# Kernel tuning notes

Hardware: AMD Instinct MI355X
Metric: run time of the kernel (lower is better)

The kernel has to match this reference:

```python
import jax, jax.numpy as jnp
import numpy as np

D_STATE = 16

def setup_inputs() -> dict:
    key = jax.random.key(0)
    ks = jax.random.split(key, 7)
    B, L, d_model = 2, 4096, 1024
    d_inner, d_conv, d_state = 2048, 4, D_STATE
    s = 0.02
    return {
        "x": jax.random.normal(ks[0], (B, L, d_model), jnp.float32),
        "W_in": jax.random.normal(ks[1], (2 * d_inner, d_model), jnp.float32) * s,
        "conv_w": jax.random.normal(ks[2], (d_inner, d_conv), jnp.float32) * 0.3,
        "conv_b": jax.random.normal(ks[3], (d_inner,), jnp.float32) * 0.1,
        "W_xproj": jax.random.normal(ks[4], (2 * d_state + d_inner, d_inner), jnp.float32) * s,
        "D": jnp.ones((d_inner,), jnp.float32),
        "W_out": jax.random.normal(ks[5], (d_model, d_inner), jnp.float32) * s,
    }

def _silu(v):
    return v * jax.nn.sigmoid(v)

def reference(x, W_in, conv_w, conv_b, W_xproj, D, W_out):
    Bsz, L, _ = x.shape
    d_inner, d_conv = conv_w.shape
    d_state = D_STATE
    # in_proj -> split into x branch and gate z
    xz = jnp.einsum('bld,ed->ble', x, W_in)           # [B,L,2*d_inner]
    xb, z = xz[..., :d_inner], xz[..., d_inner:]
    # causal depthwise conv1d (left pad d_conv-1, truncate to L)
    xpad = jnp.pad(xb, ((0, 0), (d_conv - 1, 0), (0, 0)))
    xc = conv_b
    for k in range(d_conv):  # tiny fixed kernel loop
        xc = xc + conv_w[:, k] * xpad[:, k:k + L, :]
    xc = _silu(xc)                                    # [B,L,d_inner]
    # x_proj -> B, C, delta
    proj = jnp.einsum('bld,ed->ble', xc, W_xproj)     # [B,L,2*d_state+d_inner]
    Bm = proj[..., :d_state]
    Cm = proj[..., d_state:2 * d_state]
    delta = jax.nn.softplus(proj[..., 2 * d_state:])  # [B,L,d_inner]
    # selective 'scan' as written collapses: y[b,l,d] = delta*x * sum_s B*C + D*x
    bc = jnp.einsum('bls,bls->bl', Bm, Cm)            # [B,L]
    y = delta * xc * bc[..., None] + D * xc
    y = y * _silu(z)
    return jnp.einsum('bld,ed->ble', y, W_out)        # [B,L,d_model]
```

## Files before the change

kernel.cpp:

```cpp
#include <hip/hip_runtime.h>
#include <hip/hip_bf16.h>
#include <cstdint>
#include <cmath>

typedef __bf16 bf16x8 __attribute__((ext_vector_type(8)));
typedef float  f32x4  __attribute__((ext_vector_type(4)));
typedef unsigned short u16x8 __attribute__((ext_vector_type(8)));

#define BT 128
#define BK 64

__device__ __forceinline__ float bf2f(unsigned short h) {
  union { unsigned int u; float f; } v; v.u = ((unsigned int)h) << 16;
  return v.f;
}
__device__ __forceinline__ unsigned short f2bf(float x) {
  union { float f; unsigned int u; } v; v.f = x;
  unsigned int r = v.u + 0x7fffu + ((v.u >> 16) & 1u);
  return (unsigned short)(r >> 16);
}

__device__ __forceinline__ void gld_lds16(const void* g, void* l) {
  __builtin_amdgcn_global_load_lds(
      (const __attribute__((address_space(1))) unsigned int*)g,
      (__attribute__((address_space(3))) unsigned int*)l,
      16, 0, 0);
}

__device__ __forceinline__ void cvt4(const float* __restrict__ in,
                                     unsigned short* __restrict__ out, int i) {
  float4 v = reinterpret_cast<const float4*>(in)[i];
  ushort4 o;
  o.x = f2bf(v.x); o.y = f2bf(v.y); o.z = f2bf(v.z); o.w = f2bf(v.w);
  reinterpret_cast<ushort4*>(out)[i] = o;
}

__global__ void cvt_head(const float* __restrict__ x, unsigned short* __restrict__ xb,
                         const float* __restrict__ W_in, unsigned short* __restrict__ wb) {
  int b = blockIdx.x;
  if (b < 8192) cvt4(x, xb, b * 256 + threadIdx.x);
  else          cvt4(W_in, wb, (b - 8192) * 256 + threadIdx.x);
}

__device__ void conv_strip(const unsigned short* __restrict__ xz,
                           const float* __restrict__ conv_w,
                           const float* __restrict__ conv_b,
                           unsigned short* __restrict__ xc,
                           int strip, int tid) {
  const int bl0  = strip * 32;
  const int seq0 = bl0 & ~4095;
  const int c0   = tid * 8;
  float w[4][8], bb[8];
#pragma unroll
  for (int j = 0; j < 8; ++j) {
    float4 wr = reinterpret_cast<const float4*>(conv_w)[c0 + j];
    w[0][j] = wr.x; w[1][j] = wr.y; w[2][j] = wr.z; w[3][j] = wr.w;
    bb[j] = conv_b[c0 + j];
  }
  float win[3][8];
#pragma unroll
  for (int i = 0; i < 3; ++i) {
    int r = bl0 - 3 + i;
    if (r >= seq0) {
      u16x8 v = *reinterpret_cast<const u16x8*>(xz + (size_t)r * 4096 + c0);
#pragma unroll
      for (int j = 0; j < 8; ++j) win[i][j] = bf2f(v[j]);
    } else {
#pragma unroll
      for (int j = 0; j < 8; ++j) win[i][j] = 0.f;
    }
  }
  for (int i = 0; i < 32; ++i) {
    const int bl = bl0 + i;
    u16x8 v = *reinterpret_cast<const u16x8*>(xz + (size_t)bl * 4096 + c0);
    u16x8 o;
#pragma unroll
    for (int j = 0; j < 8; ++j) {
      float cur = bf2f(v[j]);
      float a = bb[j] + w[0][j] * win[0][j] + w[1][j] * win[1][j]
                      + w[2][j] * win[2][j] + w[3][j] * cur;
      o[j] = f2bf(a / (1.f + expf(-a)));
      win[0][j] = win[1][j]; win[1][j] = win[2][j]; win[2][j] = cur;
    }
    *reinterpret_cast<u16x8*>(xc + (size_t)bl * 2048 + c0) = o;
  }
}

__global__ void mid_fused(const unsigned short* __restrict__ xz,
                          const float* __restrict__ conv_w,
                          const float* __restrict__ conv_b,
                          unsigned short* __restrict__ xc,
                          const float* __restrict__ W_xproj, unsigned short* __restrict__ wx_bf,
                          const float* __restrict__ W_out,   unsigned short* __restrict__ wo_bf) {
  int b = blockIdx.x;
  if (b < 256) { conv_strip(xz, conv_w, conv_b, xc, b, threadIdx.x); return; }
  b -= 256;
  if (b < 4160) { cvt4(W_xproj, wx_bf, b * 256 + threadIdx.x); return; }
  cvt4(W_out, wo_bf, (b - 4160) * 256 + threadIdx.x);
}

template <int GUARD_N, int OUT_F32>
__global__ __launch_bounds__(256, 2)
void gemm_bt(const unsigned short* __restrict__ A,
             const unsigned short* __restrict__ B,
             void* __restrict__ Cv,
             int N, int K, int ldA, int ldB, int ldC)
{
  __shared__ __align__(16) unsigned short sA[BT * BK];
  __shared__ __align__(16) unsigned short sB[BT * BK];

  const int tid  = threadIdx.x;
  const int lane = tid & 63;
  const int wave = tid >> 6;
  const int row0 = blockIdx.x * BT;
  const int col0 = blockIdx.y * BT;

  const int wrow = (wave & 1) * 64;
  const int wcol = (wave >> 1) * 64;
  const int l15  = lane & 15;
  const int q    = lane >> 4;

  f32x4 acc[4][4];
#pragma unroll
  for (int i = 0; i < 4; ++i)
#pragma unroll
    for (int j = 0; j < 4; ++j)
      acc[i][j] = (f32x4){0.f, 0.f, 0.f, 0.f};

  const int nk = K / BK;
  for (int kt = 0; kt < nk; ++kt) {
    const int k0 = kt * BK;
#pragma unroll
    for (int t = 0; t < 4; ++t) {
      int c  = t * 256 + tid;
      int r  = c >> 3;
      int g  = c & 7;
      int gs = (g ^ (r & 7)) * 8;
      gld_lds16(A + (size_t)(row0 + r) * ldA + k0 + gs, (void*)(sA + c * 8));
      int br = col0 + r;
      if (GUARD_N) br = (br < N) ? br : (N - 1);
      gld_lds16(B + (size_t)br * ldB + k0 + gs, (void*)(sB + c * 8));
    }
    __syncthreads();

#pragma unroll
    for (int kk = 0; kk < BK; kk += 32) {
      const int grb = kk >> 3;
      bf16x8 af[4], bfr[4];
#pragma unroll
      for (int i = 0; i < 4; ++i) {
        int ar = wrow + i * 16 + l15;
        af[i] = *reinterpret_cast<const bf16x8*>(
            sA + ar * BK + (((grb + q) ^ (ar & 7)) << 3));
        int br = wcol + i * 16 + l15;
        bfr[i] = *reinterpret_cast<const bf16x8*>(
            sB + br * BK + (((grb + q) ^ (br & 7)) << 3));
      }
#pragma unroll
      for (int i = 0; i < 4; ++i)
#pragma unroll
        for (int j = 0; j < 4; ++j)
          acc[i][j] = __builtin_amdgcn_mfma_f32_16x16x32_bf16(af[i], bfr[j], acc[i][j], 0, 0, 0);
    }
    __syncthreads();
  }

#pragma unroll
  for (int i = 0; i < 4; ++i) {
#pragma unroll
    for (int j = 0; j < 4; ++j) {
      int colw = col0 + wcol + j * 16 + l15;
      if (GUARD_N && colw >= N) continue;
#pragma unroll
      for (int r = 0; r < 4; ++r) {
        int roww = row0 + wrow + i * 16 + q * 4 + r;
        if (OUT_F32)
          ((float*)Cv)[(size_t)roww * ldC + colw] = acc[i][j][r];
        else
          ((unsigned short*)Cv)[(size_t)roww * ldC + colw] = f2bf(acc[i][j][r]);
      }
    }
  }
}

#define BARX() do { __builtin_amdgcn_sched_barrier(0); \
                    __builtin_amdgcn_s_barrier(); \
                    __builtin_amdgcn_sched_barrier(0); } while (0)
#define VMW(n) asm volatile("s_waitcnt vmcnt(" #n ")" ::: "memory")

#define STAGE_A(b, h, kt) do { \
  const unsigned short* _p = Ab + (size_t)((h) * 128) * ldA + (kt) * 64; \
  gld_lds16(_p,                     (void*)&sA[b][((h) * 128      + rr) * 64 + (g8 << 3)]); \
  gld_lds16(_p + (size_t)64 * ldA,  (void*)&sA[b][((h) * 128 + 64 + rr) * 64 + (g8 << 3)]); \
} while (0)

#define STAGE_B(b, h, kt) do { \
  const unsigned short* _p = Bb + (size_t)((h) * 128) * ldB + (kt) * 64; \
  gld_lds16(_p,                     (void*)&sB[b][((h) * 128      + rr) * 64 + (g8 << 3)]); \
  gld_lds16(_p + (size_t)64 * ldB,  (void*)&sB[b][((h) * 128 + 64 + rr) * 64 + (g8 << 3)]); \
} while (0)

#define RD_A(b, p) do { \
  af[0][0] = *reinterpret_cast<const bf16x8*>(&sA[b][aOff + (2*(p)    ) * 1024 + kph0]); \
  af[0][1] = *reinterpret_cast<const bf16x8*>(&sA[b][aOff + (2*(p)    ) * 1024 + kph1]); \
  af[1][0] = *reinterpret_cast<const bf16x8*>(&sA[b][aOff + (2*(p) + 1) * 1024 + kph0]); \
  af[1][1] = *reinterpret_cast<const bf16x8*>(&sA[b][aOff + (2*(p) + 1) * 1024 + kph1]); \
} while (0)

#define RD_B(b) do { \
  bf[0][0] = *reinterpret_cast<const bf16x8*>(&sB[b][bOff + 0 * 1024 + kph0]); \
  bf[0][1] = *reinterpret_cast<const bf16x8*>(&sB[b][bOff + 0 * 1024 + kph1]); \
  bf[1][0] = *reinterpret_cast<const bf16x8*>(&sB[b][bOff + 1 * 1024 + kph0]); \
  bf[1][1] = *reinterpret_cast<const bf16x8*>(&sB[b][bOff + 1 * 1024 + kph1]); \
  bf[2][0] = *reinterpret_cast<const bf16x8*>(&sB[b][bOff + 2 * 1024 + kph0]); \
  bf[2][1] = *reinterpret_cast<const bf16x8*>(&sB[b][bOff + 2 * 1024 + kph1]); \
  bf[3][0] = *reinterpret_cast<const bf16x8*>(&sB[b][bOff + 3 * 1024 + kph0]); \
  bf[3][1] = *reinterpret_cast<const bf16x8*>(&sB[b][bOff + 3 * 1024 + kph1]); \
} while (0)

#define MM2(i, j) \
  acc[i][j] = __builtin_amdgcn_mfma_f32_16x16x32_bf16(af[(i) & 1][0], bf[j][0], acc[i][j], 0, 0, 0); \
  acc[i][j] = __builtin_amdgcn_mfma_f32_16x16x32_bf16(af[(i) & 1][1], bf[j][1], acc[i][j], 0, 0, 0)

#define MFMA_PH(p) do { \
  __builtin_amdgcn_s_setprio(1); \
  MM2(2*(p),     0); MM2(2*(p),     1); MM2(2*(p),     2); MM2(2*(p),     3); \
  MM2(2*(p) + 1, 0); MM2(2*(p) + 1, 1); MM2(2*(p) + 1, 2); MM2(2*(p) + 1, 3); \
  __builtin_amdgcn_s_setprio(0); \
} while (0)

__global__ __launch_bounds__(512, 2)
void gemm256(const unsigned short* __restrict__ A,
             const unsigned short* __restrict__ B,
             unsigned short* __restrict__ C,
             int K, int ldA, int ldB, int ldC, int nbn)
{
  __shared__ __align__(16) unsigned short sA[2][256 * 64];
  __shared__ __align__(16) unsigned short sB[2][256 * 64];

  const int tid  = threadIdx.x;
  const int lane = tid & 63;
  const int wave = tid >> 6;
  const int wm = wave >> 2;
  const int wn = wave & 3;
  const int l15 = lane & 15;
  const int q   = lane >> 4;

  const int nwg = gridDim.x;
  const int wg  = blockIdx.x;
  const int swz = (wg & 7) * (nwg >> 3) + (wg >> 3);
  const int row0 = (swz / nbn) * 256;
  const int col0 = (swz % nbn) * 256;

  const int rr  = tid >> 3;
  const int g8  = tid & 7;
  const int gsw = ((g8 ^ (rr & 7)) << 3);
  const unsigned short* Ab = A + (size_t)(row0 + rr) * ldA + gsw;
  const unsigned short* Bb = B + (size_t)(col0 + rr) * ldB + gsw;

  const int aOff = (wm * 128 + l15) * 64;
  const int bOff = (wn * 64  + l15) * 64;
  const int a7   = l15 & 7;
  const int kph0 = ((q       ^ a7) << 3);
  const int kph1 = (((4 + q) ^ a7) << 3);

  f32x4 acc[8][4];
#pragma unroll
  for (int i = 0; i < 8; ++i)
#pragma unroll
    for (int j = 0; j < 4; ++j)
      acc[i][j] = (f32x4){0.f, 0.f, 0.f, 0.f};

  bf16x8 af[2][2], bf[4][2];

  const int nk = K >> 6;
  STAGE_A(0, 0, 0); STAGE_A(0, 1, 0);
  STAGE_B(0, 0, 0); STAGE_B(0, 1, 0);
  STAGE_B(1, 0, 1); STAGE_B(1, 1, 1);
  VMW(4);
  BARX();

  const int niter = K >> 7;
  for (int it = 0; it < niter; ++it) {
    const int kt1 = 2 * it + 1;
    int ktE = 2 * it + 2; if (ktE > nk - 1) ktE = nk - 1;
    int ktO = 2 * it + 3; if (ktO > nk - 1) ktO = nk - 1;

    RD_B(0); RD_A(0, 0); STAGE_A(1, 0, kt1);
    BARX(); MFMA_PH(0); BARX();
    RD_A(0, 1); STAGE_A(1, 1, kt1);
    BARX(); MFMA_PH(1); BARX();
    RD_A(0, 2); STAGE_B(0, 0, ktE);
    BARX(); MFMA_PH(2); BARX();
    RD_A(0, 3); STAGE_B(0, 1, ktE);
    VMW(4);
    BARX(); MFMA_PH(3); BARX();

    RD_B(1); RD_A(1, 0); STAGE_A(0, 0, ktE);
    BARX(); MFMA_PH(0); BARX();
    RD_A(1, 1); STAGE_A(0, 1, ktE);
    BARX(); MFMA_PH(1); BARX();
    RD_A(1, 2); STAGE_B(1, 0, ktO);
    BARX(); MFMA_PH(2); BARX();
    RD_A(1, 3); STAGE_B(1, 1, ktO);
    VMW(4);
    BARX(); MFMA_PH(3); BARX();
  }

#pragma unroll
  for (int i = 0; i < 8; ++i) {
    const int roww = row0 + wm * 128 + i * 16 + q * 4;
#pragma unroll
    for (int j = 0; j < 4; ++j) {
      const int colw = col0 + wn * 64 + j * 16 + l15;
      unsigned short* cp = C + (size_t)roww * ldC + colw;
#pragma unroll
      for (int r = 0; r < 4; ++r)
        cp[(size_t)r * ldC] = f2bf(acc[i][j][r]);
    }
  }
}

__global__ __launch_bounds__(256)
void proj_strip(const unsigned short* __restrict__ xc,
                const unsigned short* __restrict__ wx,
                unsigned short* __restrict__ proj)
{
  __shared__ float red[4][32 * 32];
  const int tid  = threadIdx.x;
  const int lane = tid & 63;
  const int wave = tid >> 6;
  const int l15  = lane & 15;
  const int q    = lane >> 4;
  const int row0 = blockIdx.x * 32;

  f32x4 acc[2][2];
#pragma unroll
  for (int i = 0; i < 2; ++i)
#pragma unroll
    for (int j = 0; j < 2; ++j) acc[i][j] = (f32x4){0.f, 0.f, 0.f, 0.f};

  const int kbase = wave * 512;
#pragma unroll 4
  for (int kk = 0; kk < 512; kk += 32) {
    const int k = kbase + kk + q * 8;
    bf16x8 a0 = *reinterpret_cast<const bf16x8*>(&xc[(size_t)(row0 + l15) * 2048 + k]);
    bf16x8 a1 = *reinterpret_cast<const bf16x8*>(&xc[(size_t)(row0 + 16 + l15) * 2048 + k]);
    bf16x8 b0 = *reinterpret_cast<const bf16x8*>(&wx[(size_t)(l15) * 2048 + k]);
    bf16x8 b1 = *reinterpret_cast<const bf16x8*>(&wx[(size_t)(16 + l15) * 2048 + k]);
    acc[0][0] = __builtin_amdgcn_mfma_f32_16x16x32_bf16(a0, b0, acc[0][0], 0, 0, 0);
    acc[0][1] = __builtin_amdgcn_mfma_f32_16x16x32_bf16(a0, b1, acc[0][1], 0, 0, 0);
    acc[1][0] = __builtin_amdgcn_mfma_f32_16x16x32_bf16(a1, b0, acc[1][0], 0, 0, 0);
    acc[1][1] = __builtin_amdgcn_mfma_f32_16x16x32_bf16(a1, b1, acc[1][1], 0, 0, 0);
  }

#pragma unroll
  for (int i = 0; i < 2; ++i)
#pragma unroll
    for (int j = 0; j < 2; ++j)
#pragma unroll
      for (int r = 0; r < 4; ++r)
        red[wave][(i * 16 + q * 4 + r) * 32 + j * 16 + l15] = acc[i][j][r];
  __syncthreads();

#pragma unroll
  for (int t = 0; t < 4; ++t) {
    int idx = tid + t * 256;
    float s = red[0][idx] + red[1][idx] + red[2][idx] + red[3][idx];
    proj[(size_t)(row0 + (idx >> 5)) * 2080 + (idx & 31)] = f2bf(s);
  }
}

__global__ void gate_kernel(const unsigned short* __restrict__ proj,
                            const unsigned short* __restrict__ xz,
                            const float* __restrict__ Dw,
                            unsigned short* __restrict__ xc_y)
{
  const int bl = blockIdx.x;
  const unsigned short* p = proj + (size_t)bl * 2080;
  u16x8 pb0 = *reinterpret_cast<const u16x8*>(p);
  u16x8 pb1 = *reinterpret_cast<const u16x8*>(p + 8);
  u16x8 pc0 = *reinterpret_cast<const u16x8*>(p + 16);
  u16x8 pc1 = *reinterpret_cast<const u16x8*>(p + 24);
  float bc = 0.f;
#pragma unroll
  for (int s = 0; s < 8; ++s)
    bc += bf2f(pb0[s]) * bf2f(pc0[s]) + bf2f(pb1[s]) * bf2f(pc1[s]);

  const int c0 = threadIdx.x * 8;
  u16x8 dv  = *reinterpret_cast<const u16x8*>(p + 32 + c0);
  u16x8 xcv = *reinterpret_cast<const u16x8*>(xc_y + (size_t)bl * 2048 + c0);
  u16x8 zv  = *reinterpret_cast<const u16x8*>(xz + (size_t)bl * 4096 + 2048 + c0);
  float4 d0 = reinterpret_cast<const float4*>(Dw)[c0 / 4];
  float4 d1 = reinterpret_cast<const float4*>(Dw)[c0 / 4 + 1];
  const float* dd0 = reinterpret_cast<const float*>(&d0);
  const float* dd1 = reinterpret_cast<const float*>(&d1);

  u16x8 o;
#pragma unroll
  for (int j = 0; j < 8; ++j) {
    float d = bf2f(dv[j]);
    float delta = (d > 15.f) ? d : log1pf(expf(d));
    float xv = bf2f(xcv[j]);
    float z  = bf2f(zv[j]);
    float Dj = (j < 4) ? dd0[j] : dd1[j - 4];
    float y = delta * xv * bc + Dj * xv;
    y *= z / (1.f + expf(-z));
    o[j] = f2bf(y);
  }
  *reinterpret_cast<u16x8*>(xc_y + (size_t)bl * 2048 + c0) = o;
}

extern "C" void kernel_launch(void* const* d_in, const int* in_sizes, int n_in,
                              void* d_out, int out_size, void* d_ws, size_t ws_size,
                              hipStream_t stream) {
  const float* x       = (const float*)d_in[0];
  const float* W_in    = (const float*)d_in[1];
  const float* conv_w  = (const float*)d_in[2];
  const float* conv_b  = (const float*)d_in[3];
  const float* W_xproj = (const float*)d_in[4];
  const float* Dw      = (const float*)d_in[5];
  const float* W_out   = (const float*)d_in[6];
  float* out = (float*)d_out;

  unsigned short* xz_bf   = (unsigned short*)d_ws;
  unsigned short* xc_bf   = xz_bf  + (size_t)8192 * 4096;
  unsigned short* proj_bf = xc_bf  + (size_t)8192 * 2048;
  unsigned short* xb_bf   = proj_bf + (size_t)8192 * 2080;
  unsigned short* w_bf    = xb_bf  + (size_t)8192 * 1024;

  cvt_head<<<8192 + 4096, 256, 0, stream>>>(x, xb_bf, W_in, w_bf);
  gemm256<<<512, 512, 0, stream>>>(xb_bf, w_bf, xz_bf, 1024, 1024, 1024, 4096, 16);
  mid_fused<<<256 + 4160 + 2048, 256, 0, stream>>>(xz_bf, conv_w, conv_b, xc_bf,
                                                   W_xproj, xb_bf, W_out, w_bf);
  proj_strip<<<256, 256, 0, stream>>>(xc_bf, xb_bf, proj_bf);
  gemm256<<<256, 512, 0, stream>>>(xc_bf, xb_bf + (size_t)32 * 2048, proj_bf + 32,
                                   2048, 2048, 2048, 2080, 8);
  gate_kernel<<<8192, 256, 0, stream>>>(proj_bf, xz_bf, Dw, xc_bf);
  gemm_bt<0, 1><<<dim3(64, 8), 256, 0, stream>>>(xc_bf, w_bf, out, 1024, 2048, 2048, 2048, 1024);
}
```

Before: 393.4 us.

## Double-buffer MFMA register fragments to overlap LDS reads with MFMA phases

Splits the A and B register fragments into even/odd sets so that the LDS reads for the next phase are issued right after the current phase's MFMAs, rather than before them. The intent is to hide LDS read latency behind matrix math. It also reorders the MFMAs so both k-halves interleave across accumulators. This costs more VGPRs under a 512-thread, 2-block launch bound, and adds a prologue read before the loop. The final iteration's prefetch reads stale or unused data, which should be harmless.

```diff
diff --git a/kernel.cpp b/kernel.cpp
--- a/kernel.cpp
+++ b/kernel.cpp
@@ -200,32 +200,37 @@
   gld_lds16(_p + (size_t)64 * ldB,  (void*)&sB[b][((h) * 128 + 64 + rr) * 64 + (g8 << 3)]); \
 } while (0)
 
-#define RD_A(b, p) do { \
-  af[0][0] = *reinterpret_cast<const bf16x8*>(&sA[b][aOff + (2*(p)    ) * 1024 + kph0]); \
-  af[0][1] = *reinterpret_cast<const bf16x8*>(&sA[b][aOff + (2*(p)    ) * 1024 + kph1]); \
-  af[1][0] = *reinterpret_cast<const bf16x8*>(&sA[b][aOff + (2*(p) + 1) * 1024 + kph0]); \
-  af[1][1] = *reinterpret_cast<const bf16x8*>(&sA[b][aOff + (2*(p) + 1) * 1024 + kph1]); \
+#define RD_A_SET(dst, b, p) do { \
+  dst[0][0] = *reinterpret_cast<const bf16x8*>(&sA[b][aOff + (2*(p)    ) * 1024 + kph0]); \
+  dst[0][1] = *reinterpret_cast<const bf16x8*>(&sA[b][aOff + (2*(p)    ) * 1024 + kph1]); \
+  dst[1][0] = *reinterpret_cast<const bf16x8*>(&sA[b][aOff + (2*(p) + 1) * 1024 + kph0]); \
+  dst[1][1] = *reinterpret_cast<const bf16x8*>(&sA[b][aOff + (2*(p) + 1) * 1024 + kph1]); \
 } while (0)
 
-#define RD_B(b) do { \
-  bf[0][0] = *reinterpret_cast<const bf16x8*>(&sB[b][bOff + 0 * 1024 + kph0]); \
-  bf[0][1] = *reinterpret_cast<const bf16x8*>(&sB[b][bOff + 0 * 1024 + kph1]); \
-  bf[1][0] = *reinterpret_cast<const bf16x8*>(&sB[b][bOff + 1 * 1024 + kph0]); \
-  bf[1][1] = *reinterpret_cast<const bf16x8*>(&sB[b][bOff + 1 * 1024 + kph1]); \
-  bf[2][0] = *reinterpret_cast<const bf16x8*>(&sB[b][bOff + 2 * 1024 + kph0]); \
-  bf[2][1] = *reinterpret_cast<const bf16x8*>(&sB[b][bOff + 2 * 1024 + kph1]); \
-  bf[3][0] = *reinterpret_cast<const bf16x8*>(&sB[b][bOff + 3 * 1024 + kph0]); \
-  bf[3][1] = *reinterpret_cast<const bf16x8*>(&sB[b][bOff + 3 * 1024 + kph1]); \
+#define RD_B_SET(dst, b) do { \
+  dst[0][0] = *reinterpret_cast<const bf16x8*>(&sB[b][bOff + 0 * 1024 + kph0]); \
+  dst[0][1] = *reinterpret_cast<const bf16x8*>(&sB[b][bOff + 0 * 1024 + kph1]); \
+  dst[1][0] = *reinterpret_cast<const bf16x8*>(&sB[b][bOff + 1 * 1024 + kph0]); \
+  dst[1][1] = *reinterpret_cast<const bf16x8*>(&sB[b][bOff + 1 * 1024 + kph1]); \
+  dst[2][0] = *reinterpret_cast<const bf16x8*>(&sB[b][bOff + 2 * 1024 + kph0]); \
+  dst[2][1] = *reinterpret_cast<const bf16x8*>(&sB[b][bOff + 2 * 1024 + kph1]); \
+  dst[3][0] = *reinterpret_cast<const bf16x8*>(&sB[b][bOff + 3 * 1024 + kph0]); \
+  dst[3][1] = *reinterpret_cast<const bf16x8*>(&sB[b][bOff + 3 * 1024 + kph1]); \
 } while (0)
 
-#define MM2(i, j) \
-  acc[i][j] = __builtin_amdgcn_mfma_f32_16x16x32_bf16(af[(i) & 1][0], bf[j][0], acc[i][j], 0, 0, 0); \
-  acc[i][j] = __builtin_amdgcn_mfma_f32_16x16x32_bf16(af[(i) & 1][1], bf[j][1], acc[i][j], 0, 0, 0)
-
-#define MFMA_PH(p) do { \
+#define MMA(i, j, k, Af, Bf) \
+  acc[i][j] = __builtin_amdgcn_mfma_f32_16x16x32_bf16(Af[(i) & 1][k], Bf[j][k], acc[i][j], 0, 0, 0)
+
+#define MFMA_PH(p, Af, Bf) do { \
   __builtin_amdgcn_s_setprio(1); \
-  MM2(2*(p),     0); MM2(2*(p),     1); MM2(2*(p),     2); MM2(2*(p),     3); \
-  MM2(2*(p) + 1, 0); MM2(2*(p) + 1, 1); MM2(2*(p) + 1, 2); MM2(2*(p) + 1, 3); \
+  MMA(2*(p),   0, 0, Af, Bf); MMA(2*(p),   1, 0, Af, Bf); \
+  MMA(2*(p),   2, 0, Af, Bf); MMA(2*(p),   3, 0, Af, Bf); \
+  MMA(2*(p)+1, 0, 0, Af, Bf); MMA(2*(p)+1, 1, 0, Af, Bf); \
+  MMA(2*(p)+1, 2, 0, Af, Bf); MMA(2*(p)+1, 3, 0, Af, Bf); \
+  MMA(2*(p),   0, 1, Af, Bf); MMA(2*(p),   1, 1, Af, Bf); \
+  MMA(2*(p),   2, 1, Af, Bf); MMA(2*(p),   3, 1, Af, Bf); \
+  MMA(2*(p)+1, 0, 1, Af, Bf); MMA(2*(p)+1, 1, 1, Af, Bf); \
+  MMA(2*(p)+1, 2, 1, Af, Bf); MMA(2*(p)+1, 3, 1, Af, Bf); \
   __builtin_amdgcn_s_setprio(0); \
 } while (0)
 
@@ -271,7 +276,8 @@
     for (int j = 0; j < 4; ++j)
       acc[i][j] = (f32x4){0.f, 0.f, 0.f, 0.f};
 
-  bf16x8 af[2][2], bf[4][2];
+  bf16x8 afe[2][2], afo[2][2];
+  bf16x8 bfe[4][2], bfo[4][2];
 
   const int nk = K >> 6;
   STAGE_A(0, 0, 0); STAGE_A(0, 1, 0);
@@ -279,6 +285,7 @@
   STAGE_B(1, 0, 1); STAGE_B(1, 1, 1);
   VMW(4);
   BARX();
+  RD_B_SET(bfe, 0); RD_A_SET(afe, 0, 0);
 
   const int niter = K >> 7;
   for (int it = 0; it < niter; ++it) {
@@ -286,25 +293,41 @@
     int ktE = 2 * it + 2; if (ktE > nk - 1) ktE = nk - 1;
     int ktO = 2 * it + 3; if (ktO > nk - 1) ktO = nk - 1;
 
-    RD_B(0); RD_A(0, 0); STAGE_A(1, 0, kt1);
-    BARX(); MFMA_PH(0); BARX();
-    RD_A(0, 1); STAGE_A(1, 1, kt1);
-    BARX(); MFMA_PH(1); BARX();
-    RD_A(0, 2); STAGE_B(0, 0, ktE);
-    BARX(); MFMA_PH(2); BARX();
-    RD_A(0, 3); STAGE_B(0, 1, ktE);
+    STAGE_A(1, 0, kt1);
+    BARX();
+    MFMA_PH(0, afe, bfe); RD_A_SET(afo, 0, 1);
+    BARX();
+    STAGE_A(1, 1, kt1);
+    BARX();
+    MFMA_PH(1, afo, bfe); RD_A_SET(afe, 0, 2);
+    BARX();
+    STAGE_B(0, 0, ktE);
+    BARX();
+    MFMA_PH(2, afe, bfe); RD_A_SET(afo, 0, 3);
+    BARX();
+    STAGE_B(0, 1, ktE);
     VMW(4);
-    BARX(); MFMA_PH(3); BARX();
-
-    RD_B(1); RD_A(1, 0); STAGE_A(0, 0, ktE);
-    BARX(); MFMA_PH(0); BARX();
-    RD_A(1, 1); STAGE_A(0, 1, ktE);
-    BARX(); MFMA_PH(1); BARX();
-    RD_A(1, 2); STAGE_B(1, 0, ktO);
-    BARX(); MFMA_PH(2); BARX();
-    RD_A(1, 3); STAGE_B(1, 1, ktO);
+    BARX();
+    MFMA_PH(3, afo, bfe); RD_B_SET(bfo, 1); RD_A_SET(afe, 1, 0);
+    BARX();
+
+    STAGE_A(0, 0, ktE);
+    BARX();
+    MFMA_PH(0, afe, bfo); RD_A_SET(afo, 1, 1);
+    BARX();
+    STAGE_A(0, 1, ktE);
+    BARX();
+    MFMA_PH(1, afo, bfo); RD_A_SET(afe, 1, 2);
+    BARX();
+    STAGE_B(1, 0, ktO);
+    BARX();
+    MFMA_PH(2, afe, bfo); RD_A_SET(afo, 1, 3);
+    BARX();
+    STAGE_B(1, 1, ktO);
     VMW(4);
-    BARX(); MFMA_PH(3); BARX();
+    BARX();
+    MFMA_PH(3, afo, bfo); RD_B_SET(bfe, 0); RD_A_SET(afe, 0, 0);
+    BARX();
   }
 
 #pragma unroll
```

Result: no change. 398.7 us (+1.3%).
